# Optimization experiments

Hardware: AMD Instinct MI355X
Metric: run time of the kernel (lower is better)

Reference implementation:

```python
import jax, jax.numpy as jnp
import numpy as np

N_NODES = 50000
N_EDGES = 1600000
C_IN = 128
C_OUT = 128


def setup_inputs() -> dict:
    key = jax.random.key(0)
    k1, k2, k3 = jax.random.split(key, 3)
    x = jax.random.normal(k1, (N_NODES, C_IN), dtype=jnp.float32)
    edge_index = jax.random.randint(k2, (2, N_EDGES), 0, N_NODES, dtype=jnp.int64)
    # Glorot-style init for the GCN weight, zero bias (PyG defaults)
    scale = jnp.sqrt(6.0 / (C_IN + C_OUT)).astype(jnp.float32)
    W = jax.random.uniform(k3, (C_IN, C_OUT), dtype=jnp.float32, minval=-scale, maxval=scale)
    b = jnp.zeros((C_OUT,), dtype=jnp.float32)
    return {"x": x, "edge_index": edge_index, "W": W, "b": b}


def reference(x, edge_index, W, b):
    N = x.shape[0]
    # Linear transform first (PyG GCNConv applies lin before propagate)
    h = x @ W  # [N, C_OUT]

    # Add self-loops
    loop = jnp.arange(N, dtype=edge_index.dtype)
    row = jnp.concatenate([edge_index[0], loop])  # source nodes
    col = jnp.concatenate([edge_index[1], loop])  # target nodes

    # Symmetric degree normalization: deg computed at target (col)
    ones = jnp.ones(row.shape[0], dtype=h.dtype)
    deg = jax.ops.segment_sum(ones, col, num_segments=N)  # [N]
    deg_inv_sqrt = jnp.where(deg > 0, jax.lax.rsqrt(deg), 0.0)
    norm = deg_inv_sqrt[row] * deg_inv_sqrt[col]  # [E+N]

    # Gather source features, scale, scatter-add to targets
    msg = h[row] * norm[:, None]  # [E+N, C_OUT]
    out = jax.ops.segment_sum(msg, col, num_segments=N)  # [N, C_OUT]
    out = out + b
    return jax.nn.relu(out)
```

## Files before the change

kernel.cpp:

```cpp
#include <hip/hip_runtime.h>
#include <stdint.h>

#define NCH 128
#define BK_SHIFT 7
#define BK_TGTS 128
#define NBUCK_MAX 512
#define BKT_CAP 5120
#define PT_EDGES 4096
#define BS_CAP 5120

typedef short bf16x8 __attribute__((ext_vector_type(8)));
typedef float f32x4 __attribute__((ext_vector_type(4)));
typedef float f32x2 __attribute__((ext_vector_type(2)));

__device__ __forceinline__ unsigned short f2bf(float f) {
    union { float f; uint32_t u; } v; v.f = f;
    uint32_t u = v.u;
    uint32_t r = u + 0x7fffu + ((u >> 16) & 1u);
    return (unsigned short)(r >> 16);
}
__device__ __forceinline__ float bf2f(unsigned short h) {
    return __uint_as_float((uint32_t)h << 16);
}
__device__ __forceinline__ float bflo(uint32_t u) { return __uint_as_float(u << 16); }
__device__ __forceinline__ float bfhi(uint32_t u) { return __uint_as_float(u & 0xffff0000u); }
__device__ __forceinline__ f32x2 bfpair(uint32_t u) {
    f32x2 r;
    r.x = __uint_as_float(u << 16);
    r.y = __uint_as_float(u & 0xffff0000u);
    return r;
}

__global__ __launch_bounds__(256) void prep_w_kernel(const float* __restrict__ W,
                                                     short* __restrict__ whl,
                                                     int* __restrict__ bcur) {
    if (blockIdx.x == 0) {
        for (int i = threadIdx.x; i < NBUCK_MAX; i += 256) bcur[i] = 0;
    }
    const int idx = blockIdx.x * 256 + threadIdx.x;
    if (idx >= 2048) return;
    const int ko = idx >> 7;
    const int n = idx & 127;
    const int kt = ko >> 2, g = ko & 3;
    const int ct = n >> 4, l16 = n & 15;
    const int row = g * 16 + l16;
    bf16x8 vh, vl;
    #pragma unroll
    for (int e = 0; e < 8; ++e) {
        const float w = W[(size_t)(ko * 8 + e) * NCH + n];
        const unsigned short wh = f2bf(w);
        vh[e] = (short)wh;
        vl[e] = (short)f2bf(w - bf2f(wh));
    }
    *reinterpret_cast<bf16x8*>(&whl[(((0 * 4 + kt) * 8 + ct) * 64 + row) * 8]) = vh;
    *reinterpret_cast<bf16x8*>(&whl[(((1 * 4 + kt) * 8 + ct) * 64 + row) * 8]) = vl;
}

__global__ __launch_bounds__(256) void partition_kernel(const int* __restrict__ ei, int E,
                                                        int nbuck,
                                                        int* __restrict__ bcur,
                                                        uint32_t* __restrict__ bkt) {
    __shared__ int hist[NBUCK_MAX];
    __shared__ int cbase[NBUCK_MAX];
    __shared__ uint32_t stage[PT_EDGES];
    __shared__ int s_is64;
    const int t = threadIdx.x;
    const int e0 = blockIdx.x * PT_EDGES;
    const int cnt = min(PT_EDGES, E - e0);

    if (t == 0) s_is64 = 0;
    for (int i = t; i < NBUCK_MAX; i += 256) hist[i] = 0;
    __syncthreads();
    if (t < 128 && ei[2 * t + 1] != 0) s_is64 = 1;
    __syncthreads();
    const bool is64 = (s_is64 == 0);

    int rank[PT_EDGES / 256];
    #pragma unroll
    for (int j = 0; j < PT_EDGES / 256; ++j) {
        const int i = t + j * 256;
        if (i < cnt) {
            int r, c;
            if (is64) {
                r = reinterpret_cast<const int2*>(ei)[(size_t)(e0 + i)].x;
                c = reinterpret_cast<const int2*>(ei)[(size_t)E + e0 + i].x;
            } else {
                r = ei[e0 + i];
                c = ei[(size_t)E + e0 + i];
            }
            stage[i] = ((uint32_t)c << 16) | (uint32_t)r;
            rank[j] = atomicAdd(&hist[c >> BK_SHIFT], 1);
        }
    }
    __syncthreads();
    for (int b = t; b < nbuck; b += 256) {
        cbase[b] = hist[b] ? atomicAdd(&bcur[b], hist[b]) : 0;
    }
    __syncthreads();
    #pragma unroll
    for (int j = 0; j < PT_EDGES / 256; ++j) {
        const int i = t + j * 256;
        if (i < cnt) {
            const uint32_t p = stage[i];
            const int b = (int)(p >> (16 + BK_SHIFT));
            const int pos = cbase[b] + rank[j];
            if (pos < BKT_CAP) bkt[(size_t)b * BKT_CAP + pos] = p;
        }
    }
}

__global__ __launch_bounds__(256) void bucket_sort_kernel(const uint32_t* __restrict__ bkt,
                                                          const int* __restrict__ bcur,
                                                          int N, int nbuck,
                                                          unsigned short* __restrict__ entries,
                                                          int* __restrict__ offsets,
                                                          float* __restrict__ dinv) {
    __shared__ uint32_t se[BS_CAP];
    __shared__ int hist[BK_TGTS];
    __shared__ int lofs[BK_TGTS];
    __shared__ int s_beg;
    const int b = blockIdx.x;
    const int t = threadIdx.x;
    const int c0 = b << BK_SHIFT;
    const int ntgt = min(BK_TGTS, N - c0);

    for (int i = t; i < BK_TGTS; i += 256) hist[i] = 0;
    if (t < 64) {
        int sum = 0;
        for (int i = t; i < b; i += 64) sum += min(bcur[i], BKT_CAP);
        #pragma unroll
        for (int d = 1; d < 64; d <<= 1) sum += __shfl_xor(sum, d);
        if (t == 0) s_beg = sum;
    }
    __syncthreads();
    const int beg = s_beg;
    const int nE = min(bcur[b], BKT_CAP);
    const int nE4 = nE & ~3;
    const uint32_t* win = bkt + (size_t)b * BKT_CAP;

    for (int i = t * 4; i < nE4; i += 1024) {
        const uint4 p = *reinterpret_cast<const uint4*>(win + i);
        *reinterpret_cast<uint4*>(&se[i]) = p;
        atomicAdd(&hist[(int)(p.x >> 16) - c0], 1);
        atomicAdd(&hist[(int)(p.y >> 16) - c0], 1);
        atomicAdd(&hist[(int)(p.z >> 16) - c0], 1);
        atomicAdd(&hist[(int)(p.w >> 16) - c0], 1);
    }
    for (int i = nE4 + t; i < nE; i += 256) {
        const uint32_t p = win[i];
        se[i] = p;
        atomicAdd(&hist[(int)(p >> 16) - c0], 1);
    }
    __syncthreads();

    if (t < 64) {
        const int h0 = hist[2 * t], h1 = hist[2 * t + 1];
        int s = h0 + h1;
        #pragma unroll
        for (int d = 1; d < 64; d <<= 1) {
            const int u = __shfl_up(s, d);
            if (t >= d) s += u;
        }
        const int ex = s - (h0 + h1);
        lofs[2 * t] = ex;
        lofs[2 * t + 1] = ex + h0;
    }
    __syncthreads();

    for (int i = t; i < ntgt; i += 256) {
        offsets[c0 + i] = beg + lofs[i];
        dinv[c0 + i] = rsqrtf((float)(hist[i] + 1));
    }
    if (t == 0 && b == nbuck - 1) offsets[N] = beg + nE;
    __syncthreads();

    for (int i = t; i < BK_TGTS; i += 256) hist[i] = lofs[i];
    __syncthreads();
    for (int i = t * 4; i < nE4; i += 1024) {
        const uint4 p = *reinterpret_cast<const uint4*>(&se[i]);
        int pos;
        pos = atomicAdd(&hist[(int)(p.x >> 16) - c0], 1); entries[beg + pos] = (unsigned short)(p.x & 0xffffu);
        pos = atomicAdd(&hist[(int)(p.y >> 16) - c0], 1); entries[beg + pos] = (unsigned short)(p.y & 0xffffu);
        pos = atomicAdd(&hist[(int)(p.z >> 16) - c0], 1); entries[beg + pos] = (unsigned short)(p.z & 0xffffu);
        pos = atomicAdd(&hist[(int)(p.w >> 16) - c0], 1); entries[beg + pos] = (unsigned short)(p.w & 0xffffu);
    }
    for (int i = nE4 + t; i < nE; i += 256) {
        const uint32_t p = se[i];
        const int pos = atomicAdd(&hist[(int)(p >> 16) - c0], 1);
        entries[beg + pos] = (unsigned short)(p & 0xffffu);
    }
}

__global__ __launch_bounds__(256) void gemm_xw_mfma_kernel(const float* __restrict__ x,
                                                           const short* __restrict__ whl,
                                                           const float* __restrict__ dinv,
                                                           uint32_t* __restrict__ hb, int N) {
    __shared__ short sW[2][4][8][64][8];
    const int t = threadIdx.x;

    {
        short* d = &sW[0][0][0][0][0];
        #pragma unroll
        for (int i = t * 8; i < 2 * 4 * 8 * 64 * 8; i += 256 * 8)
            *reinterpret_cast<bf16x8*>(d + i) = *reinterpret_cast<const bf16x8*>(whl + i);
    }
    __syncthreads();

    const int wave = t >> 6;
    const int lane = t & 63;
    const int g = lane >> 4;
    const int l16 = lane & 15;
    const int row0 = blockIdx.x * 128 + wave * 16;
    if (row0 >= N) return;

    bf16x8 ah[2][4], al[2][4];
    float dn[2][4];
    #pragma unroll
    for (int grp = 0; grp < 2; ++grp) {
        const int rbase = row0 + grp * 64;
        const int arow = min(rbase + l16, N - 1);
        const float* xr = x + (size_t)arow * NCH + g * 8;
        #pragma unroll
        for (int kt = 0; kt < 4; ++kt) {
            const float4 v0 = *reinterpret_cast<const float4*>(xr + kt * 32);
            const float4 v1 = *reinterpret_cast<const float4*>(xr + kt * 32 + 4);
            const float vv[8] = {v0.x, v0.y, v0.z, v0.w, v1.x, v1.y, v1.z, v1.w};
            #pragma unroll
            for (int e = 0; e < 8; ++e) {
                const unsigned short h16 = f2bf(vv[e]);
                ah[grp][kt][e] = (short)h16;
                al[grp][kt][e] = (short)f2bf(vv[e] - bf2f(h16));
            }
        }
        #pragma unroll
        for (int r = 0; r < 4; ++r) dn[grp][r] = dinv[min(rbase + g * 4 + r, N - 1)];
    }

    #pragma unroll
    for (int ct = 0; ct < 8; ++ct) {
        f32x4 accA = {0.f, 0.f, 0.f, 0.f};
        f32x4 accB = {0.f, 0.f, 0.f, 0.f};
        #pragma unroll
        for (int kt = 0; kt < 4; ++kt) {
            const bf16x8 bh = *reinterpret_cast<const bf16x8*>(&sW[0][kt][ct][lane][0]);
            const bf16x8 bl = *reinterpret_cast<const bf16x8*>(&sW[1][kt][ct][lane][0]);
            accA = __builtin_amdgcn_mfma_f32_16x16x32_bf16(ah[0][kt], bh, accA, 0, 0, 0);
            accA = __builtin_amdgcn_mfma_f32_16x16x32_bf16(al[0][kt], bh, accA, 0, 0, 0);
            accA = __builtin_amdgcn_mfma_f32_16x16x32_bf16(ah[0][kt], bl, accA, 0, 0, 0);
            accB = __builtin_amdgcn_mfma_f32_16x16x32_bf16(ah[1][kt], bh, accB, 0, 0, 0);
            accB = __builtin_amdgcn_mfma_f32_16x16x32_bf16(al[1][kt], bh, accB, 0, 0, 0);
            accB = __builtin_amdgcn_mfma_f32_16x16x32_bf16(ah[1][kt], bl, accB, 0, 0, 0);
        }
        #pragma unroll
        for (int grp = 0; grp < 2; ++grp) {
            const f32x4 acc = grp ? accB : accA;
            #pragma unroll
            for (int r = 0; r < 4; ++r) {
                const float v = acc[r] * dn[grp][r];
                const float o = __shfl_xor(v, 1);
                const int wrow = row0 + grp * 64 + g * 4 + r;
                if ((lane & 1) == 0 && wrow < N) {
                    const uint32_t p = (uint32_t)f2bf(v) | ((uint32_t)f2bf(o) << 16);
                    hb[(size_t)wrow * (NCH / 2) + ct * 8 + (l16 >> 1)] = p;
                }
            }
        }
    }
}

__global__ __launch_bounds__(256) void spmm_csr_kernel(const uint32_t* __restrict__ hb,
                                                       const unsigned short* __restrict__ entries,
                                                       const int* __restrict__ offsets,
                                                       const float* __restrict__ dinv,
                                                       const float* __restrict__ bias,
                                                       float* __restrict__ out, int N) {
    const int lane = threadIdx.x & 63;
    const int n = blockIdx.x * 4 + (threadIdx.x >> 6);
    if (n >= N) return;

    const int half = lane >> 5;
    const int sl = lane & 31;

    const int beg = offsets[n];
    const int end = offsets[n + 1];
    const int len = end - beg;
    const int cnt0 = min(len, 64);

    int pre = 0;
    if (beg + lane < end) pre = (int)__builtin_nontemporal_load(entries + beg + lane);

    const uint32_t* __restrict__ hbs = hb + sl * 2;
    f32x2 acc01 = {0.f, 0.f};
    f32x2 acc23 = {0.f, 0.f};

    int j = 0;
    for (; 2 * j + 16 <= cnt0; j += 8) {
        const int i0 = 2 * j + half;
        const int s0 = __shfl(pre, i0);
        const int s1 = __shfl(pre, i0 + 2);
        const int s2 = __shfl(pre, i0 + 4);
        const int s3 = __shfl(pre, i0 + 6);
        const int s4 = __shfl(pre, i0 + 8);
        const int s5 = __shfl(pre, i0 + 10);
        const int s6 = __shfl(pre, i0 + 12);
        const int s7 = __shfl(pre, i0 + 14);
        const uint2 u0 = *reinterpret_cast<const uint2*>(hbs + (size_t)s0 * (NCH / 2));
        const uint2 u1 = *reinterpret_cast<const uint2*>(hbs + (size_t)s1 * (NCH / 2));
        const uint2 u2 = *reinterpret_cast<const uint2*>(hbs + (size_t)s2 * (NCH / 2));
        const uint2 u3 = *reinterpret_cast<const uint2*>(hbs + (size_t)s3 * (NCH / 2));
        const uint2 u4 = *reinterpret_cast<const uint2*>(hbs + (size_t)s4 * (NCH / 2));
        const uint2 u5 = *reinterpret_cast<const uint2*>(hbs + (size_t)s5 * (NCH / 2));
        const uint2 u6 = *reinterpret_cast<const uint2*>(hbs + (size_t)s6 * (NCH / 2));
        const uint2 u7 = *reinterpret_cast<const uint2*>(hbs + (size_t)s7 * (NCH / 2));
        acc01 += bfpair(u0.x); acc23 += bfpair(u0.y);
        acc01 += bfpair(u1.x); acc23 += bfpair(u1.y);
        acc01 += bfpair(u2.x); acc23 += bfpair(u2.y);
        acc01 += bfpair(u3.x); acc23 += bfpair(u3.y);
        acc01 += bfpair(u4.x); acc23 += bfpair(u4.y);
        acc01 += bfpair(u5.x); acc23 += bfpair(u5.y);
        acc01 += bfpair(u6.x); acc23 += bfpair(u6.y);
        acc01 += bfpair(u7.x); acc23 += bfpair(u7.y);
    }
    for (; 2 * j + 8 <= cnt0; j += 4) {
        const int i0 = 2 * j + half;
        const int s0 = __shfl(pre, i0);
        const int s1 = __shfl(pre, i0 + 2);
        const int s2 = __shfl(pre, i0 + 4);
        const int s3 = __shfl(pre, i0 + 6);
        const uint2 u0 = *reinterpret_cast<const uint2*>(hbs + (size_t)s0 * (NCH / 2));
        const uint2 u1 = *reinterpret_cast<const uint2*>(hbs + (size_t)s1 * (NCH / 2));
        const uint2 u2 = *reinterpret_cast<const uint2*>(hbs + (size_t)s2 * (NCH / 2));
        const uint2 u3 = *reinterpret_cast<const uint2*>(hbs + (size_t)s3 * (NCH / 2));
        acc01 += bfpair(u0.x); acc23 += bfpair(u0.y);
        acc01 += bfpair(u1.x); acc23 += bfpair(u1.y);
        acc01 += bfpair(u2.x); acc23 += bfpair(u2.y);
        acc01 += bfpair(u3.x); acc23 += bfpair(u3.y);
    }
    for (; 2 * j < cnt0; ++j) {
        const int i0 = 2 * j + half;
        const int s0 = __shfl(pre, min(i0, 63));
        uint2 u0 = *reinterpret_cast<const uint2*>(hbs + (size_t)s0 * (NCH / 2));
        if (i0 >= cnt0) { u0.x = 0u; u0.y = 0u; }
        acc01 += bfpair(u0.x); acc23 += bfpair(u0.y);
    }
    for (int jj = beg + 64 + half; jj < end; jj += 2) {
        const int s0 = __builtin_nontemporal_load(entries + jj);
        const uint2 u0 = *reinterpret_cast<const uint2*>(hbs + (size_t)s0 * (NCH / 2));
        acc01 += bfpair(u0.x); acc23 += bfpair(u0.y);
    }

    float a0 = acc01.x, a1 = acc01.y, a2 = acc23.x, a3 = acc23.y;
    a0 += __shfl_xor(a0, 32);
    a1 += __shfl_xor(a1, 32);
    a2 += __shfl_xor(a2, 32);
    a3 += __shfl_xor(a3, 32);

    const uint2 us = *reinterpret_cast<const uint2*>(hbs + (size_t)n * (NCH / 2));
    a0 += bflo(us.x); a1 += bfhi(us.x); a2 += bflo(us.y); a3 += bfhi(us.y);

    const float s = dinv[n];
    if (half == 0) {
        const float4 bb = reinterpret_cast<const float4*>(bias)[sl];
        f32x4 o;
        o.x = fmaxf(a0 * s + bb.x, 0.f);
        o.y = fmaxf(a1 * s + bb.y, 0.f);
        o.z = fmaxf(a2 * s + bb.z, 0.f);
        o.w = fmaxf(a3 * s + bb.w, 0.f);
        __builtin_nontemporal_store(o, reinterpret_cast<f32x4*>(out + (size_t)n * NCH + sl * 4));
    }
}

extern "C" void kernel_launch(void* const* d_in, const int* in_sizes, int n_in,
                              void* d_out, int out_size, void* d_ws, size_t ws_size,
                              hipStream_t stream) {
    const float* x = (const float*)d_in[0];
    const int* ei = (const int*)d_in[1];
    const float* W = (const float*)d_in[2];
    const float* bias = (const float*)d_in[3];
    float* out = (float*)d_out;

    const int N = in_sizes[0] / NCH;
    const int E = in_sizes[1] / 2;
    const int nbuck = (N + BK_TGTS - 1) >> BK_SHIFT;

    char* w = (char*)d_ws;
    const int padN = (N + 127) & ~127;
    const int padN1 = (N + 1 + 127) & ~127;
    int* offsets = (int*)w;                 w += (size_t)padN1 * 4;
    float* dinv = (float*)w;                w += (size_t)padN * 4;
    int* bcur = (int*)w;                    w += NBUCK_MAX * 4;
    short* whl = (short*)w;                 w += 65536;
    uint32_t* bkt = (uint32_t*)w;
    uint32_t* hb = (uint32_t*)w;            w += (size_t)N * (NCH / 2) * 4;
    unsigned short* entries = (unsigned short*)w;  w += (size_t)E * 2;
    (void)ws_size;

    prep_w_kernel<<<8, 256, 0, stream>>>(W, whl, bcur);
    partition_kernel<<<(E + PT_EDGES - 1) / PT_EDGES, 256, 0, stream>>>(ei, E, nbuck, bcur, bkt);
    bucket_sort_kernel<<<nbuck, 256, 0, stream>>>(bkt, bcur, N, nbuck, entries, offsets, dinv);
    gemm_xw_mfma_kernel<<<(N + 127) / 128, 256, 0, stream>>>(x, whl, dinv, hb, N);
    spmm_csr_kernel<<<(N + 3) / 4, 256, 0, stream>>>(hb, entries, offsets, dinv, bias, out, N);
}
```

Before: 109.4 us.

## Split bf16 feature matrix into channel-sliced planes for cache-local SpMM gathers

```diff
diff --git a/kernel.cpp b/kernel.cpp
--- a/kernel.cpp
+++ b/kernel.cpp
@@ -8,6 +8,8 @@
 #define BKT_CAP 5120
 #define PT_EDGES 4096
 #define BS_CAP 5120
+#define NSLICE 4
+#define PL_U32 16
 
 typedef short bf16x8 __attribute__((ext_vector_type(8)));
 typedef float f32x4 __attribute__((ext_vector_type(4)));
@@ -251,6 +253,8 @@
             accB = __builtin_amdgcn_mfma_f32_16x16x32_bf16(al[1][kt], bh, accB, 0, 0, 0);
             accB = __builtin_amdgcn_mfma_f32_16x16x32_bf16(ah[1][kt], bl, accB, 0, 0, 0);
         }
+        const int plane = ct >> 1;
+        const int pidx = (ct & 1) * 8 + (l16 >> 1);
         #pragma unroll
         for (int grp = 0; grp < 2; ++grp) {
             const f32x4 acc = grp ? accB : accA;
@@ -261,25 +265,25 @@
                 const int wrow = row0 + grp * 64 + g * 4 + r;
                 if ((lane & 1) == 0 && wrow < N) {
                     const uint32_t p = (uint32_t)f2bf(v) | ((uint32_t)f2bf(o) << 16);
-                    hb[(size_t)wrow * (NCH / 2) + ct * 8 + (l16 >> 1)] = p;
+                    hb[((size_t)plane * N + wrow) * PL_U32 + pidx] = p;
                 }
             }
         }
     }
 }
 
-__global__ __launch_bounds__(256) void spmm_csr_kernel(const uint32_t* __restrict__ hb,
-                                                       const unsigned short* __restrict__ entries,
-                                                       const int* __restrict__ offsets,
-                                                       const float* __restrict__ dinv,
-                                                       const float* __restrict__ bias,
-                                                       float* __restrict__ out, int N) {
+__global__ __launch_bounds__(256) void spmm_sliced_kernel(const uint32_t* __restrict__ hb,
+                                                          const unsigned short* __restrict__ entries,
+                                                          const int* __restrict__ offsets,
+                                                          const float* __restrict__ dinv,
+                                                          const float* __restrict__ bias,
+                                                          float* __restrict__ out, int N) {
+    const int slice = blockIdx.x & 3;
+    const int n = (blockIdx.x >> 2) * 4 + (threadIdx.x >> 6);
+    if (n >= N) return;
     const int lane = threadIdx.x & 63;
-    const int n = blockIdx.x * 4 + (threadIdx.x >> 6);
-    if (n >= N) return;
-
-    const int half = lane >> 5;
-    const int sl = lane & 31;
+    const int g = lane >> 4;
+    const int c = lane & 15;
 
     const int beg = offsets[n];
     const int end = offsets[n + 1];
@@ -289,84 +293,48 @@
     int pre = 0;
     if (beg + lane < end) pre = (int)__builtin_nontemporal_load(entries + beg + lane);
 
-    const uint32_t* __restrict__ hbs = hb + sl * 2;
-    f32x2 acc01 = {0.f, 0.f};
-    f32x2 acc23 = {0.f, 0.f};
-
-    int j = 0;
-    for (; 2 * j + 16 <= cnt0; j += 8) {
-        const int i0 = 2 * j + half;
+    const uint32_t* __restrict__ hbs = hb + (size_t)slice * N * PL_U32 + c;
+
+    f32x2 acc = {0.f, 0.f};
+    int k = 0;
+    for (; k + 16 <= cnt0; k += 16) {
+        const int i0 = k + g;
         const int s0 = __shfl(pre, i0);
-        const int s1 = __shfl(pre, i0 + 2);
-        const int s2 = __shfl(pre, i0 + 4);
-        const int s3 = __shfl(pre, i0 + 6);
-        const int s4 = __shfl(pre, i0 + 8);
-        const int s5 = __shfl(pre, i0 + 10);
-        const int s6 = __shfl(pre, i0 + 12);
-        const int s7 = __shfl(pre, i0 + 14);
-        const uint2 u0 = *reinterpret_cast<const uint2*>(hbs + (size_t)s0 * (NCH / 2));
-        const uint2 u1 = *reinterpret_cast<const uint2*>(hbs + (size_t)s1 * (NCH / 2));
-        const uint2 u2 = *reinterpret_cast<const uint2*>(hbs + (size_t)s2 * (NCH / 2));
-        const uint2 u3 = *reinterpret_cast<const uint2*>(hbs + (size_t)s3 * (NCH / 2));
-        const uint2 u4 = *reinterpret_cast<const uint2*>(hbs + (size_t)s4 * (NCH / 2));
-        const uint2 u5 = *reinterpret_cast<const uint2*>(hbs + (size_t)s5 * (NCH / 2));
-        const uint2 u6 = *reinterpret_cast<const uint2*>(hbs + (size_t)s6 * (NCH / 2));
-        const uint2 u7 = *reinterpret_cast<const uint2*>(hbs + (size_t)s7 * (NCH / 2));
-        acc01 += bfpair(u0.x); acc23 += bfpair(u0.y);
-        acc01 += bfpair(u1.x); acc23 += bfpair(u1.y);
-        acc01 += bfpair(u2.x); acc23 += bfpair(u2.y);
-        acc01 += bfpair(u3.x); acc23 += bfpair(u3.y);
-        acc01 += bfpair(u4.x); acc23 += bfpair(u4.y);
-        acc01 += bfpair(u5.x); acc23 += bfpair(u5.y);
-        acc01 += bfpair(u6.x); acc23 += bfpair(u6.y);
-        acc01 += bfpair(u7.x); acc23 += bfpair(u7.y);
-    }
-    for (; 2 * j + 8 <= cnt0; j += 4) {
-        const int i0 = 2 * j + half;
-        const int s0 = __shfl(pre, i0);
-        const int s1 = __shfl(pre, i0 + 2);
-        const int s2 = __shfl(pre, i0 + 4);
-        const int s3 = __shfl(pre, i0 + 6);
-        const uint2 u0 = *reinterpret_cast<const uint2*>(hbs + (size_t)s0 * (NCH / 2));
-        const uint2 u1 = *reinterpret_cast<const uint2*>(hbs + (size_t)s1 * (NCH / 2));
-        const uint2 u2 = *reinterpret_cast<const uint2*>(hbs + (size_t)s2 * (NCH / 2));
-        const uint2 u3 = *reinterpret_cast<const uint2*>(hbs + (size_t)s3 * (NCH / 2));
-        acc01 += bfpair(u0.x); acc23 += bfpair(u0.y);
-        acc01 += bfpair(u1.x); acc23 += bfpair(u1.y);
-        acc01 += bfpair(u2.x); acc23 += bfpair(u2.y);
-        acc01 += bfpair(u3.x); acc23 += bfpair(u3.y);
-    }
-    for (; 2 * j < cnt0; ++j) {
-        const int i0 = 2 * j + half;
+        const int s1 = __shfl(pre, i0 + 4);
+        const int s2 = __shfl(pre, i0 + 8);
+        const int s3 = __shfl(pre, i0 + 12);
+        const uint32_t u0 = hbs[(size_t)s0 * PL_U32];
+        const uint32_t u1 = hbs[(size_t)s1 * PL_U32];
+        const uint32_t u2 = hbs[(size_t)s2 * PL_U32];
+        const uint32_t u3 = hbs[(size_t)s3 * PL_U32];
+        acc += bfpair(u0);
+        acc += bfpair(u1);
+        acc += bfpair(u2);
+        acc += bfpair(u3);
+    }
+    for (; k < cnt0; k += 4) {
+        const int i0 = k + g;
         const int s0 = __shfl(pre, min(i0, 63));
-        uint2 u0 = *reinterpret_cast<const uint2*>(hbs + (size_t)s0 * (NCH / 2));
-        if (i0 >= cnt0) { u0.x = 0u; u0.y = 0u; }
-        acc01 += bfpair(u0.x); acc23 += bfpair(u0.y);
-    }
-    for (int jj = beg + 64 + half; jj < end; jj += 2) {
-        const int s0 = __builtin_nontemporal_load(entries + jj);
-        const uint2 u0 = *reinterpret_cast<const uint2*>(hbs + (size_t)s0 * (NCH / 2));
-        acc01 += bfpair(u0.x); acc23 += bfpair(u0.y);
-    }
-
-    float a0 = acc01.x, a1 = acc01.y, a2 = acc23.x, a3 = acc23.y;
-    a0 += __shfl_xor(a0, 32);
-    a1 += __shfl_xor(a1, 32);
-    a2 += __shfl_xor(a2, 32);
-    a3 += __shfl_xor(a3, 32);
-
-    const uint2 us = *reinterpret_cast<const uint2*>(hbs + (size_t)n * (NCH / 2));
-    a0 += bflo(us.x); a1 += bfhi(us.x); a2 += bflo(us.y); a3 += bfhi(us.y);
-
-    const float s = dinv[n];
-    if (half == 0) {
-        const float4 bb = reinterpret_cast<const float4*>(bias)[sl];
-        f32x4 o;
-        o.x = fmaxf(a0 * s + bb.x, 0.f);
-        o.y = fmaxf(a1 * s + bb.y, 0.f);
-        o.z = fmaxf(a2 * s + bb.z, 0.f);
-        o.w = fmaxf(a3 * s + bb.w, 0.f);
-        __builtin_nontemporal_store(o, reinterpret_cast<f32x4*>(out + (size_t)n * NCH + sl * 4));
+        uint32_t u0 = hbs[(size_t)s0 * PL_U32];
+        if (i0 >= cnt0) u0 = 0u;
+        acc += bfpair(u0);
+    }
+    for (int jj = beg + 64 + g; jj < end; jj += 4) {
+        const int s0 = (int)__builtin_nontemporal_load(entries + jj);
+        acc += bfpair(hbs[(size_t)s0 * PL_U32]);
+    }
+
+    acc.x += __shfl_xor(acc.x, 16); acc.y += __shfl_xor(acc.y, 16);
+    acc.x += __shfl_xor(acc.x, 32); acc.y += __shfl_xor(acc.y, 32);
+
+    if (g == 0) {
+        const f32x2 sv = bfpair(hbs[(size_t)n * PL_U32]);
+        const float s = dinv[n];
+        const float2 bb = *reinterpret_cast<const float2*>(bias + slice * 32 + c * 2);
+        f32x2 o;
+        o.x = fmaxf((acc.x + sv.x) * s + bb.x, 0.f);
+        o.y = fmaxf((acc.y + sv.y) * s + bb.y, 0.f);
+        __builtin_nontemporal_store(o, reinterpret_cast<f32x2*>(out + (size_t)n * NCH + slice * 32 + c * 2));
     }
 }
 
@@ -399,5 +367,5 @@
     partition_kernel<<<(E + PT_EDGES - 1) / PT_EDGES, 256, 0, stream>>>(ei, E, nbuck, bcur, bkt);
     bucket_sort_kernel<<<nbuck, 256, 0, stream>>>(bkt, bcur, N, nbuck, entries, offsets, dinv);
     gemm_xw_mfma_kernel<<<(N + 127) / 128, 256, 0, stream>>>(x, whl, dinv, hb, N);
-    spmm_csr_kernel<<<(N + 3) / 4, 256, 0, stream>>>(hb, entries, offsets, dinv, bias, out, N);
-}
+    spmm_sliced_kernel<<<((N + 3) / 4) * 4, 256, 0, stream>>>(hb, entries, offsets, dinv, bias, out, N);
+}
```

New measurement: 153.5 us. 1.4x slower.
